# Kernel optimization log

Measured on AMD Instinct MI355X. Metric: run time of the kernel, lower is better.

The kernel has to match this reference:

```python
import jax, jax.numpy as jnp
import numpy as np

G, A = 1024, 20          # graphs, atoms per graph
N = G * A                # nodes = 20480
E = G * A * A            # fc edges within each graph = 409600
H = 128                  # hidden_dim
LATENT = 256             # latent_dim
L = 4                    # num_layers
NFREQ = 10
DIS_DIM = NFREQ * 2 * 3  # 60
EDGE_IN = 2 * H + 9 + DIS_DIM  # 325
MAX_ATOMS = 100


def _lin(k, fin, fout):
    return jax.random.normal(k, (fin, fout), dtype=jnp.float32) / np.sqrt(fin).astype(np.float32)


def _stack_lin(k, fin, fout):
    return jnp.stack([_lin(jax.random.fold_in(k, i), fin, fout) for i in range(L)])


def setup_inputs() -> dict:
    key = jax.random.key(0)
    ks = jax.random.split(key, 16)
    atom_types = jax.random.randint(ks[0], (N,), 0, MAX_ATOMS, dtype=jnp.int32)
    frac_coords = jax.random.uniform(ks[1], (N, 3), dtype=jnp.float32)
    lattices = jax.random.normal(ks[2], (G, 3, 3), dtype=jnp.float32)
    t = jax.random.normal(ks[3], (G, LATENT), dtype=jnp.float32)
    # fully-connected (fc) edges within each graph, block-diagonal structure
    base = np.arange(A)
    src = np.repeat(base, A)
    dst = np.tile(base, A)
    offs = (np.arange(G) * A)[:, None]
    edge_index = jnp.asarray(np.stack([
        (src[None, :] + offs).reshape(-1),
        (dst[None, :] + offs).reshape(-1)]), dtype=jnp.int32)  # [2, E]
    edge2graph = jnp.asarray(np.repeat(np.arange(G), A * A), dtype=jnp.int32)
    node2graph = jnp.asarray(np.repeat(np.arange(G), A), dtype=jnp.int32)
    # parameters
    emb_table = jax.random.normal(ks[4], (MAX_ATOMS, H), dtype=jnp.float32) * 0.02
    w_latent = _lin(ks[5], H + LATENT, H)
    b_latent = jnp.zeros((H,), jnp.float32)
    edge_w1 = _stack_lin(ks[6], EDGE_IN, H)
    edge_b1 = jnp.zeros((L, H), jnp.float32)
    edge_w2 = _stack_lin(ks[7], H, H)
    edge_b2 = jnp.zeros((L, H), jnp.float32)
    node_w1 = _stack_lin(ks[8], 2 * H, H)
    node_b1 = jnp.zeros((L, H), jnp.float32)
    node_w2 = _stack_lin(ks[9], H, H)
    node_b2 = jnp.zeros((L, H), jnp.float32)
    coord_w = _lin(ks[10], H, 3)
    lattice_w = _lin(ks[11], H, 9)
    return dict(atom_types=atom_types, frac_coords=frac_coords, lattices=lattices, t=t,
                edge_index=edge_index, edge2graph=edge2graph, node2graph=node2graph,
                emb_table=emb_table, w_latent=w_latent, b_latent=b_latent,
                edge_w1=edge_w1, edge_b1=edge_b1, edge_w2=edge_w2, edge_b2=edge_b2,
                node_w1=node_w1, node_b1=node_b1, node_w2=node_w2, node_b2=node_b2,
                coord_w=coord_w, lattice_w=lattice_w)


def reference(atom_types, frac_coords, lattices, t, edge_index, edge2graph, node2graph,
              emb_table, w_latent, b_latent,
              edge_w1, edge_b1, edge_w2, edge_b2,
              node_w1, node_b1, node_w2, node_b2,
              coord_w, lattice_w):
    silu = jax.nn.silu
    src, dst = edge_index[0], edge_index[1]
    # node embedding + latent conditioning
    h = emb_table[atom_types]                               # [N,H]
    h = jnp.concatenate([h, t[node2graph]], axis=1) @ w_latent + b_latent  # [N,H]
    # sinusoidal distance embedding of periodic frac diff (detached in original)
    frac_diff = (frac_coords[dst] - frac_coords[src]) % 1.0  # [E,3]
    freqs = 2.0 * jnp.pi * jnp.arange(NFREQ, dtype=frac_coords.dtype)
    emb = (frac_diff[..., None] * freqs).reshape(-1, 3 * NFREQ)
    dis = jax.lax.stop_gradient(jnp.concatenate([jnp.sin(emb), jnp.cos(emb)], axis=-1))  # [E,60]
    # lattice inner products, broadcast to edges (ip=True)
    lat_ip = jnp.einsum('gij,gkj->gik', lattices, lattices).reshape(-1, 9)
    lat_edges = lat_ip[edge2graph]                          # [E,9]
    # per-node edge counts for scatter-mean
    counts = jax.ops.segment_sum(jnp.ones_like(src, dtype=h.dtype), src, num_segments=N)
    inv_counts = (1.0 / jnp.maximum(counts, 1.0))[:, None]
    for i in range(L):
        e_in = jnp.concatenate([h[src], h[dst], lat_edges, dis], axis=1)  # [E,325]
        ef = silu(e_in @ edge_w1[i] + edge_b1[i])
        ef = silu(ef @ edge_w2[i] + edge_b2[i])               # [E,H]
        agg = jax.ops.segment_sum(ef, src, num_segments=N) * inv_counts   # scatter-mean
        n_in = jnp.concatenate([h, agg], axis=1)              # [N,2H]
        nf = silu(n_in @ node_w1[i] + node_b1[i])
        nf = silu(nf @ node_w2[i] + node_b2[i])
        h = h + nf                                            # residual
    coord_out = h @ coord_w                                   # [N,3]
    gcounts = jax.ops.segment_sum(jnp.ones((h.shape[0],), h.dtype), node2graph, num_segments=G)
    graph_feat = jax.ops.segment_sum(h, node2graph, num_segments=G) / gcounts[:, None]
    lattice_out = (graph_feat @ lattice_w).reshape(-1, 3, 3)
    lattice_out = jnp.einsum('bij,bjk->bik', lattice_out, lattices)  # ip=True
    return lattice_out, coord_out
```

## Files before the change

kernel.cpp:

```cpp
#include <hip/hip_runtime.h>
#include <stdint.h>


#define NA 20
#define HH 128

typedef unsigned short U16;
typedef unsigned int   U32;
typedef __attribute__((ext_vector_type(8))) short bf8;
typedef __attribute__((ext_vector_type(4))) float f4;

__device__ __forceinline__ float bf2f(U16 u){ return __uint_as_float(((U32)u)<<16); }
__device__ __forceinline__ U16 f2bf(float f){
    return (U16)((__float_as_uint(f) + 0x8000u) >> 16);
}
__device__ __forceinline__ float silu_f(float x){ return x/(1.0f+__expf(-x)); }
template<bool BF>
__device__ __forceinline__ float ldf(const void* p, long i){
    return BF ? bf2f(((const U16*)p)[i]) : ((const float*)p)[i];
}
__device__ __forceinline__ f4 mfma(bf8 a, bf8 b, f4 c){
    return __builtin_amdgcn_mfma_f32_16x16x32_bf16(a,b,c,0,0,0);
}
__device__ __forceinline__ bf8 ldsA(const U16* base, int stride, int row0,
                                    int kbase, int lrow, int quad){
    return *(const bf8*)(base + (row0+lrow)*stride + kbase + quad*8);
}
template<bool BF, bool WS>
__device__ __forceinline__ bf8 getB(const U16* wsb, long wbase, int kt, int nt,
                                    int lane, const void* W, long gbase, int N,
                                    int col, int kbase, int kmax, int quad){
    if constexpr(WS){
        return *(const bf8*)(wsb + wbase + (((long)kt*8 + nt)*64 + lane)*8);
    } else {
        bf8 b; int ks0 = kbase + quad*8;
#pragma unroll
        for(int j=0;j<8;j++){
            int k=ks0+j; U16 v=0;
            if(k<kmax) v = BF ? ((const U16*)W)[gbase+(long)k*N+col]
                              : f2bf(((const float*)W)[gbase+(long)k*N+col]);
            b[j]=(short)v;
        }
        return b;
    }
}

#define WS_LBASE(L) (49152 + (long)(L)*106496)
#define REPACK_BYTES 950272

__global__ __launch_bounds__(256) void repack(
    const void* wlat, const void* ew1, const void* ew2,
    const void* nw1p, const void* nw2p, const void* lat, U16* out)
{
    __shared__ int sG[4];
    const int tid=threadIdx.x;
    {
        const U16* l16=(const U16*)lat; int good=0;
#pragma unroll
        for(int u=0;u<32;u++){
            U16 x=l16[tid*32+u]; int e=(x>>7)&0xFF; good+=(e>=100&&e<=150)?1:0;
        }
#pragma unroll
        for(int o=32;o>0;o>>=1) good+=__shfl_xor(good,o);
        if((tid&63)==0) sG[tid>>6]=good;
    }
    __syncthreads();
    const bool bf = (sG[0]+sG[1]+sG[2]+sG[3]) > 6144;

    const void* W; long srow; int segk; long dst;
    const int ktg=blockIdx.x;
    if(ktg<12){ W=wlat; srow=(long)ktg*32; segk=32; dst=(long)ktg*4096; }
    else{
        int r=ktg-12, L=r/26, lk=r-26*L;
        dst = 49152 + (long)L*106496 + (long)lk*4096;
        if(lk<4)      { W=ew1;  srow=(long)L*325+lk*32;          segk=32; }
        else if(lk<8) { W=ew1;  srow=(long)L*325+128+(lk-4)*32;  segk=32; }
        else if(lk<10){ W=ew1;  srow=(long)L*325+265+(lk-8)*32;  segk=60-(lk-8)*32; }
        else if(lk<14){ W=ew2;  srow=(long)L*128+(lk-10)*32;     segk=32; }
        else if(lk<22){ W=nw1p; srow=(long)L*256+(lk-14)*32;     segk=32; }
        else          { W=nw2p; srow=(long)L*128+(lk-22)*32;     segk=32; }
    }
    for(int o=tid;o<4096;o+=256){
        int nt=o>>9, lane=(o>>3)&63, j=o&7;
        int kk=((lane>>4)<<3)+j, col=nt*16+(lane&15);
        U16 v=0;
        if(kk<segk){
            long idx=(srow+kk)*128+col;
            v = bf ? ((const U16*)W)[idx] : f2bf(((const float*)W)[idx]);
        }
        out[dst+o]=v;
    }
}

#define PB_OFF 8960
#define QB_OFF 11520
#define DB_OFF 14080
#define EB_OFF 19840

__device__ __forceinline__ void stage_dis(U16* dB, const float* tb, int ch, int tid){
    const float2* t2=(const float2*)tb;
#pragma unroll
    for(int it=0; it<5; ++it){
        int p = tid + it*512;
        int r = p>>5, j = p&31;
        if(j<30){
            int s = ch*4 + (r&3), d = r>>2;
            float2 vs = t2[s*30+j];
            float2 vd = t2[d*30+j];
            dB[r*72+j]    = f2bf(vd.x*vs.y - vd.y*vs.x);
            dB[r*72+j+30] = f2bf(vd.y*vs.y + vd.x*vs.x);
        }
    }
}

template<bool BF, bool WS>
__device__ void body(U16* sm, float* red, float* tb, float* Rall,
    const U16* wsb, int g, int tid,
    const int* __restrict__ atype, const void* frac, const void* lattices,
    const void* t, const void* emb, const void* wlat, const void* blat,
    const void* ew1, const void* eb1, const void* ew2, const void* eb2,
    const void* nw1p, const void* nb1, const void* nw2p, const void* nb2,
    const void* coordw, const void* latw, void* outv)
{
    const int lane=tid&63, w=tid>>6, lrow=lane&15, quad=lane>>4;
    const int c = w*16 + lrow;
    U16* HA=sm; U16* pB=sm+PB_OFF; U16* qB=sm+QB_OFF;
    U16* dB=sm+DB_OFF; U16* eB=sm+EB_OFF;
    U16* k1A=eB;
    float* tvecF=(float*)dB;

    for(int q=tid;q<2560;q+=512){
        int n=q>>7, cc=q&127;
        k1A[n*136+cc] = BF ? ((const U16*)emb)[(long)atype[g*NA+n]*HH+cc]
                           : f2bf(((const float*)emb)[(long)atype[g*NA+n]*HH+cc]);
    }
    for(int q=tid;q<600;q+=512){
        int n=q/30, jj=q-n*30;
        int dim=jj/10, f=jj-dim*10;
        float x = ldf<BF>(frac,(long)(g*NA+n)*3+dim);
        float rev = __builtin_amdgcn_fractf((float)f*x);
        float2 sc;
        sc.x=__builtin_amdgcn_sinf(rev);
        sc.y=__builtin_amdgcn_cosf(rev);
        ((float2*)tb)[q]=sc;
    }
    {
        int sl=tid>>7, j=tid&127; float acc=0.f;
        for(int kk=0;kk<64;kk++){
            int k=sl*64+kk;
            acc += ldf<BF>(t,(long)g*256+k)*ldf<BF>(wlat,(long)(HH+k)*HH+j);
        }
        tvecF[sl*128+j]=acc;
    }
    {
        int L=tid>>7, j=tid&127;
        float la[9];
#pragma unroll
        for(int m2=0;m2<9;m2++) la[m2]=ldf<BF>(lattices,(long)g*9+m2);
        float Rv=ldf<BF>(eb1,(long)L*HH+j);
        const long e1=(long)L*325*HH;
#pragma unroll
        for(int a2=0;a2<3;a2++)
#pragma unroll
        for(int b3=0;b3<3;b3++){
            float ip=0.f;
#pragma unroll
            for(int c2=0;c2<3;c2++) ip+=la[a2*3+c2]*la[b3*3+c2];
            Rv += ip*ldf<BF>(ew1, e1+(long)(256+a2*3+b3)*HH+j);
        }
        Rall[L*128+j]=Rv;
    }
    __syncthreads();
    {
        f4 a0={0.f,0.f,0.f,0.f}, a1={0.f,0.f,0.f,0.f};
#pragma unroll
        for(int ks=0;ks<4;ks++){
            bf8 b=getB<BF,WS>(wsb,0,ks,w,lane, wlat,0,HH,c,ks*32,128,quad);
            bf8 v0=ldsA(k1A,136,0,ks*32,lrow,quad);
            bf8 v1=ldsA(k1A,136,16,ks*32,lrow,quad);
            a0=mfma(v0,b,a0); a1=mfma(v1,b,a1);
        }
        float bias=ldf<BF>(blat,c)+tvecF[c]+tvecF[128+c]+tvecF[256+c]+tvecF[384+c];
#pragma unroll
        for(int r=0;r<4;r++){
            HA[(quad*4+r)*280+c]   =f2bf(a0[r]+bias);
            HA[(16+quad*4+r)*280+c]=f2bf(a1[r]+bias);
        }
    }
    __syncthreads();
    if(tid<320) dB[(tid>>2)*72+60+(tid&3)]=0;

    for(int L=0;L<4;L++){
        const long e1=(long)L*325*HH;
        const long LB=WS_LBASE(L);
        const int dir=L&1;
        {
            f4 p0={0.f,0.f,0.f,0.f}, p1={0.f,0.f,0.f,0.f};
            f4 q0={0.f,0.f,0.f,0.f}, q1={0.f,0.f,0.f,0.f};
#pragma unroll
            for(int ks=0;ks<4;ks++){
                bf8 bp=getB<BF,WS>(wsb,LB,      ks,w,lane, ew1,e1,       HH,c,ks*32,128,quad);
                bf8 bq=getB<BF,WS>(wsb,LB+16384,ks,w,lane, ew1,e1+128*HH,HH,c,ks*32,128,quad);
                bf8 v0=ldsA(HA,280,0,ks*32,lrow,quad);
                bf8 v1=ldsA(HA,280,16,ks*32,lrow,quad);
                p0=mfma(v0,bp,p0); p1=mfma(v1,bp,p1);
                q0=mfma(v0,bq,q0); q1=mfma(v1,bq,q1);
            }
            float Rc=Rall[L*128+c];
#pragma unroll
            for(int r=0;r<4;r++){
                int r0=quad*4+r, r1=16+quad*4+r;
                if(r0<20){ pB[r0*HH+c]=f2bf(p0[r]+Rc); qB[r0*HH+c]=f2bf(q0[r]); }
                if(r1<20){ pB[r1*HH+c]=f2bf(p1[r]+Rc); qB[r1*HH+c]=f2bf(q1[r]); }
            }
        }
        bf8 w1d0=getB<BF,WS>(wsb,LB+32768,0,w,lane, ew1,e1+(long)265*HH,HH,c,0, 60,quad);
        bf8 w1d1=getB<BF,WS>(wsb,LB+32768,1,w,lane, ew1,e1+(long)265*HH,HH,c,32,60,quad);
        bf8 w2f[4];
#pragma unroll
        for(int ks=0;ks<4;ks++)
            w2f[ks]=getB<BF,WS>(wsb,LB+40960,ks,w,lane, ew2,(long)L*HH*HH,HH,c,ks*32,128,quad);
        const float b2=ldf<BF>(eb2,(long)L*HH+c);
        if(L==0) stage_dis(dB,tb,0,tid);
        __syncthreads();

        for(int i=0;i<5;i++){
            const int ch = dir ? 4-i : i;
            float pv[4];
#pragma unroll
            for(int r=0;r<4;r++) pv[r]=bf2f(pB[(ch*4+r)*HH+c]);
#pragma unroll
            for(int m=0;m<5;m++){
                f4 a={0.f,0.f,0.f,0.f};
                __builtin_amdgcn_s_setprio(1);
                bf8 v0=ldsA(dB,72,m*16,0, lrow,quad);
                bf8 v1=ldsA(dB,72,m*16,32,lrow,quad);
                a=mfma(v0,w1d0,a); a=mfma(v1,w1d1,a);
                __builtin_amdgcn_s_setprio(0);
                float qd=bf2f(qB[(m*4+quad)*HH+c]);
#pragma unroll
                for(int r=0;r<4;r++){
                    int row=m*16+quad*4+r;
                    eB[row*136+c]=f2bf(silu_f(a[r]+pv[r]+qd));
                }
            }
            __syncthreads();
            if(i<4) stage_dis(dB,tb, dir?3-i:i+1, tid);
            float part[4]={0.f,0.f,0.f,0.f};
#pragma unroll
            for(int m=0;m<5;m++){
                f4 a={0.f,0.f,0.f,0.f};
                __builtin_amdgcn_s_setprio(1);
#pragma unroll
                for(int ks=0;ks<4;ks++){
                    bf8 v=ldsA(eB,136,m*16,ks*32,lrow,quad);
                    a=mfma(v,w2f[ks],a);
                }
                __builtin_amdgcn_s_setprio(0);
#pragma unroll
                for(int r=0;r<4;r++) part[r]+=silu_f(a[r]+b2);
            }
#pragma unroll
            for(int r=0;r<4;r++){
                float v=part[r];
                v+=__shfl_xor(v,16); v+=__shfl_xor(v,32);
                part[r]=v;
            }
            if(quad==0){
#pragma unroll
                for(int r=0;r<4;r++)
                    HA[(ch*4+r)*280+128+c]=f2bf(part[r]*0.05f);
            }
            __syncthreads();
        }
        {
            f4 a0={0.f,0.f,0.f,0.f}, a1={0.f,0.f,0.f,0.f};
#pragma unroll
            for(int ks=0;ks<8;ks++){
                bf8 b=getB<BF,WS>(wsb,LB+57344,ks,w,lane, nw1p,(long)L*256*HH,HH,c,ks*32,256,quad);
                bf8 v0=ldsA(HA,280,0,ks*32,lrow,quad);
                bf8 v1=ldsA(HA,280,16,ks*32,lrow,quad);
                a0=mfma(v0,b,a0); a1=mfma(v1,b,a1);
            }
            float n1=ldf<BF>(nb1,(long)L*HH+c);
#pragma unroll
            for(int r=0;r<4;r++){
                eB[(quad*4+r)*136+c]   =f2bf(silu_f(a0[r]+n1));
                eB[(16+quad*4+r)*136+c]=f2bf(silu_f(a1[r]+n1));
            }
        }
        __syncthreads();
        {
            f4 a0={0.f,0.f,0.f,0.f}, a1={0.f,0.f,0.f,0.f};
#pragma unroll
            for(int ks=0;ks<4;ks++){
                bf8 b=getB<BF,WS>(wsb,LB+90112,ks,w,lane, nw2p,(long)L*HH*HH,HH,c,ks*32,128,quad);
                bf8 v0=ldsA(eB,136,0,ks*32,lrow,quad);
                bf8 v1=ldsA(eB,136,16,ks*32,lrow,quad);
                a0=mfma(v0,b,a0); a1=mfma(v1,b,a1);
            }
            float n2=ldf<BF>(nb2,(long)L*HH+c);
#pragma unroll
            for(int r=0;r<4;r++){
                int r0=quad*4+r, r1=16+quad*4+r;
                HA[r0*280+c]=f2bf(bf2f(HA[r0*280+c])+silu_f(a0[r]+n2));
                HA[r1*280+c]=f2bf(bf2f(HA[r1*280+c])+silu_f(a1[r]+n2));
            }
        }
        __syncthreads();
    }

    {
        int o=tid>>3, l8=tid&7;
        float acc=0.f;
        int n=o/3, cc=o-n*3;
        if(o<60){
#pragma unroll
            for(int k8=0;k8<16;k8++){
                int k=l8*16+k8;
                acc += bf2f(HA[n*280+k]) * ldf<BF>(coordw,(long)k*3+cc);
            }
        }
        acc+=__shfl_xor(acc,1); acc+=__shfl_xor(acc,2); acc+=__shfl_xor(acc,4);
        if(o<60 && l8==0){
            if(BF) ((U16*)outv)[(long)1024*9+(long)(g*NA+n)*3+cc]=f2bf(acc);
            else   ((float*)outv)[(long)1024*9+(long)(g*NA+n)*3+cc]=acc;
        }
    }
    if(tid<HH){
        float s2=0.f;
        for(int n=0;n<NA;n++) s2+=bf2f(HA[n*280+tid]);
        red[tid]=s2*0.05f;
    }
    __syncthreads();
    {
        int o=tid>>4, l16=tid&15;
        float acc=0.f;
        if(o<9){
#pragma unroll
            for(int k8=0;k8<8;k8++){
                int k=l16*8+k8;
                acc += red[k]*ldf<BF>(latw,(long)k*9+o);
            }
        }
        acc+=__shfl_xor(acc,1); acc+=__shfl_xor(acc,2);
        acc+=__shfl_xor(acc,4); acc+=__shfl_xor(acc,8);
        if(o<9 && l16==0) red[HH+o]=acc;
    }
    __syncthreads();
    if(tid<9){
        int i2=tid/3, k2=tid-(tid/3)*3; float acc=0.f;
#pragma unroll
        for(int j3=0;j3<3;j3++)
            acc+=red[HH+i2*3+j3]*ldf<BF>(lattices,(long)g*9+j3*3+k2);
        if(BF) ((U16*)outv)[(long)g*9+tid]=f2bf(acc);
        else   ((float*)outv)[(long)g*9+tid]=acc;
    }
}

template<bool WS>
__device__ void mega_impl(const U16* wsb,
    const int* atype, const void* frac, const void* lattices, const void* t,
    const void* emb, const void* wlat, const void* blat,
    const void* ew1, const void* eb1, const void* ew2, const void* eb2,
    const void* nw1p, const void* nb1, const void* nw2p, const void* nb2,
    const void* coordw, const void* latw, void* outv)
{
    __shared__ __align__(16) unsigned char smraw[68928];
    U16* sm = (U16*)smraw;
    float* red = (float*)(smraw+61440);
    float* tb  = (float*)(smraw+62080);
    float* Rall= (float*)(smraw+66880);
    const int g=blockIdx.x, tid=threadIdx.x, w=tid>>6, lane=tid&63;
    int* di=(int*)red;
    {
        const U16* l16=(const U16*)lattices; int good=0;
#pragma unroll
        for(int u=0;u<16;u++){
            U16 x=l16[tid*16+u]; int e=(x>>7)&0xFF; good+=(e>=100&&e<=150)?1:0;
        }
#pragma unroll
        for(int o=32;o>0;o>>=1) good+=__shfl_xor(good,o);
        if(lane==0) di[w]=good;
    }
    __syncthreads();
    if(tid==0){ int s=0; for(int i=0;i<8;i++) s+=di[i]; di[8]=(s>6144)?1:0; }
    __syncthreads();
    const int bfm=di[8];
    __syncthreads();
    if(bfm) body<true ,WS>(sm,red,tb,Rall,wsb,g,tid,atype,frac,lattices,t,emb,wlat,blat,
                           ew1,eb1,ew2,eb2,nw1p,nb1,nw2p,nb2,coordw,latw,outv);
    else    body<false,WS>(sm,red,tb,Rall,wsb,g,tid,atype,frac,lattices,t,emb,wlat,blat,
                           ew1,eb1,ew2,eb2,nw1p,nb1,nw2p,nb2,coordw,latw,outv);
}

__global__ __launch_bounds__(512,2) void mega_ws(const U16* wsb,
    const int* atype, const void* frac, const void* lattices, const void* t,
    const void* emb, const void* wlat, const void* blat,
    const void* ew1, const void* eb1, const void* ew2, const void* eb2,
    const void* nw1p, const void* nb1, const void* nw2p, const void* nb2,
    const void* coordw, const void* latw, void* outv)
{
    mega_impl<true>(wsb,atype,frac,lattices,t,emb,wlat,blat,ew1,eb1,ew2,eb2,
                    nw1p,nb1,nw2p,nb2,coordw,latw,outv);
}

__global__ __launch_bounds__(512,2) void mega_direct(const U16* wsb,
    const int* atype, const void* frac, const void* lattices, const void* t,
    const void* emb, const void* wlat, const void* blat,
    const void* ew1, const void* eb1, const void* ew2, const void* eb2,
    const void* nw1p, const void* nb1, const void* nw2p, const void* nb2,
    const void* coordw, const void* latw, void* outv)
{
    mega_impl<false>(wsb,atype,frac,lattices,t,emb,wlat,blat,ew1,eb1,ew2,eb2,
                     nw1p,nb1,nw2p,nb2,coordw,latw,outv);
}

extern "C" void kernel_launch(void* const* d_in, const int* in_sizes, int n_in,
                              void* d_out, int out_size, void* d_ws, size_t ws_size,
                              hipStream_t stream)
{
    (void)in_sizes; (void)n_in; (void)out_size;
    const int* atype = (const int*)d_in[0];
    if(ws_size >= REPACK_BYTES){
        repack<<<116, 256, 0, stream>>>(d_in[8], d_in[10], d_in[12], d_in[14],
                                        d_in[16], d_in[2], (U16*)d_ws);
        mega_ws<<<1024, 512, 0, stream>>>((const U16*)d_ws,
            atype, d_in[1], d_in[2], d_in[3], d_in[7], d_in[8], d_in[9],
            d_in[10], d_in[11], d_in[12], d_in[13], d_in[14], d_in[15],
            d_in[16], d_in[17], d_in[18], d_in[19], d_out);
    } else {
        mega_direct<<<1024, 512, 0, stream>>>(nullptr,
            atype, d_in[1], d_in[2], d_in[3], d_in[7], d_in[8], d_in[9],
            d_in[10], d_in[11], d_in[12], d_in[13], d_in[14], d_in[15],
            d_in[16], d_in[17], d_in[18], d_in[19], d_out);
    }
}
```

Before: 397.3 us.

## Keep p/q projections in registers and halve edge buffer to raise occupancy

Removes the pB/qB LDS staging buffers, keeping per-node projections in registers and distributing them with cross-lane shuffles. The 80-row edge tile per chunk is split into two sub-tiles of 48 and 32 rows so the eB buffer shrinks, cutting shared memory from about 69KB to about 50KB. Launch bounds are raised from 2 to 6 blocks per SIMD group to allow more resident blocks. In exchange the kernel adds barriers and shuffles per chunk, and the tighter register budget risks spills.

```diff
diff --git a/kernel.cpp b/kernel.cpp
--- a/kernel.cpp
+++ b/kernel.cpp
@@ -92,10 +92,8 @@
     }
 }
 
-#define PB_OFF 8960
-#define QB_OFF 11520
-#define DB_OFF 14080
-#define EB_OFF 19840
+#define DB_OFF 8960
+#define EB_OFF 14720
 
 __device__ __forceinline__ void stage_dis(U16* dB, const float* tb, int ch, int tid){
     const float2* t2=(const float2*)tb;
@@ -124,8 +122,7 @@
 {
     const int lane=tid&63, w=tid>>6, lrow=lane&15, quad=lane>>4;
     const int c = w*16 + lrow;
-    U16* HA=sm; U16* pB=sm+PB_OFF; U16* qB=sm+QB_OFF;
-    U16* dB=sm+DB_OFF; U16* eB=sm+EB_OFF;
+    U16* HA=sm; U16* dB=sm+DB_OFF; U16* eB=sm+EB_OFF;
     U16* k1A=eB;
     float* tvecF=(float*)dB;
 
@@ -194,6 +191,7 @@
         const long e1=(long)L*325*HH;
         const long LB=WS_LBASE(L);
         const int dir=L&1;
+        float p0f[4],p1f[4],q0f[4],q1f[4];
         {
             f4 p0={0.f,0.f,0.f,0.f}, p1={0.f,0.f,0.f,0.f};
             f4 q0={0.f,0.f,0.f,0.f}, q1={0.f,0.f,0.f,0.f};
@@ -209,10 +207,21 @@
             float Rc=Rall[L*128+c];
 #pragma unroll
             for(int r=0;r<4;r++){
-                int r0=quad*4+r, r1=16+quad*4+r;
-                if(r0<20){ pB[r0*HH+c]=f2bf(p0[r]+Rc); qB[r0*HH+c]=f2bf(q0[r]); }
-                if(r1<20){ pB[r1*HH+c]=f2bf(p1[r]+Rc); qB[r1*HH+c]=f2bf(q1[r]); }
-            }
+                p0f[r]=p0[r]+Rc; p1f[r]=p1[r]+Rc;
+                q0f[r]=q0[r];    q1f[r]=q1[r];
+            }
+        }
+        float qreg[5];
+#pragma unroll
+        for(int m=0;m<4;m++){
+            float t0=__shfl(q0f[0], m*16+lrow), t1=__shfl(q0f[1], m*16+lrow);
+            float t2=__shfl(q0f[2], m*16+lrow), t3=__shfl(q0f[3], m*16+lrow);
+            qreg[m] = (quad&2) ? ((quad&1)?t3:t2) : ((quad&1)?t1:t0);
+        }
+        {
+            float t0=__shfl(q1f[0], lrow), t1=__shfl(q1f[1], lrow);
+            float t2=__shfl(q1f[2], lrow), t3=__shfl(q1f[3], lrow);
+            qreg[4] = (quad&2) ? ((quad&1)?t3:t2) : ((quad&1)?t1:t0);
         }
         bf8 w1d0=getB<BF,WS>(wsb,LB+32768,0,w,lane, ew1,e1+(long)265*HH,HH,c,0, 60,quad);
         bf8 w1d1=getB<BF,WS>(wsb,LB+32768,1,w,lane, ew1,e1+(long)265*HH,HH,c,32,60,quad);
@@ -221,23 +230,28 @@
         for(int ks=0;ks<4;ks++)
             w2f[ks]=getB<BF,WS>(wsb,LB+40960,ks,w,lane, ew2,(long)L*HH*HH,HH,c,ks*32,128,quad);
         const float b2=ldf<BF>(eb2,(long)L*HH+c);
-        if(L==0) stage_dis(dB,tb,0,tid);
-        __syncthreads();
+        if(L==0){ stage_dis(dB,tb,0,tid); __syncthreads(); }
 
         for(int i=0;i<5;i++){
             const int ch = dir ? 4-i : i;
             float pv[4];
-#pragma unroll
-            for(int r=0;r<4;r++) pv[r]=bf2f(pB[(ch*4+r)*HH+c]);
-#pragma unroll
-            for(int m=0;m<5;m++){
+            if(ch<4){
+#pragma unroll
+                for(int r=0;r<4;r++) pv[r]=__shfl(p0f[r], ch*16+lrow);
+            } else {
+#pragma unroll
+                for(int r=0;r<4;r++) pv[r]=__shfl(p1f[r], lrow);
+            }
+            float part[4]={0.f,0.f,0.f,0.f};
+#pragma unroll
+            for(int m=0;m<3;m++){
                 f4 a={0.f,0.f,0.f,0.f};
                 __builtin_amdgcn_s_setprio(1);
                 bf8 v0=ldsA(dB,72,m*16,0, lrow,quad);
                 bf8 v1=ldsA(dB,72,m*16,32,lrow,quad);
                 a=mfma(v0,w1d0,a); a=mfma(v1,w1d1,a);
                 __builtin_amdgcn_s_setprio(0);
-                float qd=bf2f(qB[(m*4+quad)*HH+c]);
+                float qd=qreg[m];
 #pragma unroll
                 for(int r=0;r<4;r++){
                     int row=m*16+quad*4+r;
@@ -245,10 +259,8 @@
                 }
             }
             __syncthreads();
-            if(i<4) stage_dis(dB,tb, dir?3-i:i+1, tid);
-            float part[4]={0.f,0.f,0.f,0.f};
-#pragma unroll
-            for(int m=0;m<5;m++){
+#pragma unroll
+            for(int m=0;m<3;m++){
                 f4 a={0.f,0.f,0.f,0.f};
                 __builtin_amdgcn_s_setprio(1);
 #pragma unroll
@@ -260,6 +272,37 @@
 #pragma unroll
                 for(int r=0;r<4;r++) part[r]+=silu_f(a[r]+b2);
             }
+            __syncthreads();
+#pragma unroll
+            for(int m=3;m<5;m++){
+                f4 a={0.f,0.f,0.f,0.f};
+                __builtin_amdgcn_s_setprio(1);
+                bf8 v0=ldsA(dB,72,m*16,0, lrow,quad);
+                bf8 v1=ldsA(dB,72,m*16,32,lrow,quad);
+                a=mfma(v0,w1d0,a); a=mfma(v1,w1d1,a);
+                __builtin_amdgcn_s_setprio(0);
+                float qd=qreg[m];
+#pragma unroll
+                for(int r=0;r<4;r++){
+                    int row=(m-3)*16+quad*4+r;
+                    eB[row*136+c]=f2bf(silu_f(a[r]+pv[r]+qd));
+                }
+            }
+            __syncthreads();
+#pragma unroll
+            for(int m=3;m<5;m++){
+                f4 a={0.f,0.f,0.f,0.f};
+                __builtin_amdgcn_s_setprio(1);
+#pragma unroll
+                for(int ks=0;ks<4;ks++){
+                    bf8 v=ldsA(eB,136,(m-3)*16,ks*32,lrow,quad);
+                    a=mfma(v,w2f[ks],a);
+                }
+                __builtin_amdgcn_s_setprio(0);
+#pragma unroll
+                for(int r=0;r<4;r++) part[r]+=silu_f(a[r]+b2);
+            }
+            if(i<4) stage_dis(dB,tb, dir?3-i:i+1, tid);
 #pragma unroll
             for(int r=0;r<4;r++){
                 float v=part[r];
@@ -366,11 +409,11 @@
     const void* nw1p, const void* nb1, const void* nw2p, const void* nb2,
     const void* coordw, const void* latw, void* outv)
 {
-    __shared__ __align__(16) unsigned char smraw[68928];
+    __shared__ __align__(16) unsigned char smraw[49984];
     U16* sm = (U16*)smraw;
-    float* red = (float*)(smraw+61440);
-    float* tb  = (float*)(smraw+62080);
-    float* Rall= (float*)(smraw+66880);
+    float* red = (float*)(smraw+42496);
+    float* tb  = (float*)(smraw+43136);
+    float* Rall= (float*)(smraw+47936);
     const int g=blockIdx.x, tid=threadIdx.x, w=tid>>6, lane=tid&63;
     int* di=(int*)red;
     {
@@ -394,7 +437,7 @@
                            ew1,eb1,ew2,eb2,nw1p,nb1,nw2p,nb2,coordw,latw,outv);
 }
 
-__global__ __launch_bounds__(512,2) void mega_ws(const U16* wsb,
+__global__ __launch_bounds__(512,6) void mega_ws(const U16* wsb,
     const int* atype, const void* frac, const void* lattices, const void* t,
     const void* emb, const void* wlat, const void* blat,
     const void* ew1, const void* eb1, const void* ew2, const void* eb2,
@@ -405,7 +448,7 @@
                     nw1p,nb1,nw2p,nb2,coordw,latw,outv);
 }
 
-__global__ __launch_bounds__(512,2) void mega_direct(const U16* wsb,
+__global__ __launch_bounds__(512,6) void mega_direct(const U16* wsb,
     const int* atype, const void* frac, const void* lattices, const void* t,
     const void* emb, const void* wlat, const void* blat,
     const void* ew1, const void* eb1, const void* ew2, const void* eb2,
```

Result: slower. 460.0 us (+15.8%).

## Split edge chunk processing in two halves to shrink LDS footprint

Applied to the files above, without the earlier changes.

The per-chunk edge MLP now runs in two halves (3 then 2 row tiles) that reuse a smaller eB staging buffer, and the HA/pB/qB regions are trimmed to 20 rows instead of 32. Total shared memory drops from about 67KB to about 52KB. The aim is to fit more workgroups per CU for better latency hiding. The cost is two extra __syncthreads per chunk, and the next dis staging now happens later, after the second half.

```diff
diff --git a/kernel.cpp b/kernel.cpp
--- a/kernel.cpp
+++ b/kernel.cpp
@@ -92,10 +92,10 @@
     }
 }
 
-#define PB_OFF 8960
-#define QB_OFF 11520
-#define DB_OFF 14080
-#define EB_OFF 19840
+#define PB_OFF 5600
+#define QB_OFF 8160
+#define DB_OFF 10720
+#define EB_OFF 16480
 
 __device__ __forceinline__ void stage_dis(U16* dB, const float* tb, int ch, int tid){
     const float2* t2=(const float2*)tb;
@@ -183,8 +183,9 @@
         float bias=ldf<BF>(blat,c)+tvecF[c]+tvecF[128+c]+tvecF[256+c]+tvecF[384+c];
 #pragma unroll
         for(int r=0;r<4;r++){
-            HA[(quad*4+r)*280+c]   =f2bf(a0[r]+bias);
-            HA[(16+quad*4+r)*280+c]=f2bf(a1[r]+bias);
+            int r1=16+quad*4+r;
+            HA[(quad*4+r)*280+c]=f2bf(a0[r]+bias);
+            if(r1<20) HA[r1*280+c]=f2bf(a1[r]+bias);
         }
     }
     __syncthreads();
@@ -210,7 +211,7 @@
 #pragma unroll
             for(int r=0;r<4;r++){
                 int r0=quad*4+r, r1=16+quad*4+r;
-                if(r0<20){ pB[r0*HH+c]=f2bf(p0[r]+Rc); qB[r0*HH+c]=f2bf(q0[r]); }
+                pB[r0*HH+c]=f2bf(p0[r]+Rc); qB[r0*HH+c]=f2bf(q0[r]);
                 if(r1<20){ pB[r1*HH+c]=f2bf(p1[r]+Rc); qB[r1*HH+c]=f2bf(q1[r]); }
             }
         }
@@ -229,8 +230,9 @@
             float pv[4];
 #pragma unroll
             for(int r=0;r<4;r++) pv[r]=bf2f(pB[(ch*4+r)*HH+c]);
-#pragma unroll
-            for(int m=0;m<5;m++){
+            float part[4]={0.f,0.f,0.f,0.f};
+#pragma unroll
+            for(int m=0;m<3;m++){
                 f4 a={0.f,0.f,0.f,0.f};
                 __builtin_amdgcn_s_setprio(1);
                 bf8 v0=ldsA(dB,72,m*16,0, lrow,quad);
@@ -245,10 +247,8 @@
                 }
             }
             __syncthreads();
-            if(i<4) stage_dis(dB,tb, dir?3-i:i+1, tid);
-            float part[4]={0.f,0.f,0.f,0.f};
-#pragma unroll
-            for(int m=0;m<5;m++){
+#pragma unroll
+            for(int m=0;m<3;m++){
                 f4 a={0.f,0.f,0.f,0.f};
                 __builtin_amdgcn_s_setprio(1);
 #pragma unroll
@@ -260,6 +260,37 @@
 #pragma unroll
                 for(int r=0;r<4;r++) part[r]+=silu_f(a[r]+b2);
             }
+            __syncthreads();
+#pragma unroll
+            for(int m=3;m<5;m++){
+                f4 a={0.f,0.f,0.f,0.f};
+                __builtin_amdgcn_s_setprio(1);
+                bf8 v0=ldsA(dB,72,m*16,0, lrow,quad);
+                bf8 v1=ldsA(dB,72,m*16,32,lrow,quad);
+                a=mfma(v0,w1d0,a); a=mfma(v1,w1d1,a);
+                __builtin_amdgcn_s_setprio(0);
+                float qd=bf2f(qB[(m*4+quad)*HH+c]);
+#pragma unroll
+                for(int r=0;r<4;r++){
+                    int row=(m-3)*16+quad*4+r;
+                    eB[row*136+c]=f2bf(silu_f(a[r]+pv[r]+qd));
+                }
+            }
+            __syncthreads();
+#pragma unroll
+            for(int m=3;m<5;m++){
+                f4 a={0.f,0.f,0.f,0.f};
+                __builtin_amdgcn_s_setprio(1);
+#pragma unroll
+                for(int ks=0;ks<4;ks++){
+                    bf8 v=ldsA(eB,136,(m-3)*16,ks*32,lrow,quad);
+                    a=mfma(v,w2f[ks],a);
+                }
+                __builtin_amdgcn_s_setprio(0);
+#pragma unroll
+                for(int r=0;r<4;r++) part[r]+=silu_f(a[r]+b2);
+            }
+            if(i<4) stage_dis(dB,tb, dir?3-i:i+1, tid);
 #pragma unroll
             for(int r=0;r<4;r++){
                 float v=part[r];
@@ -304,7 +335,7 @@
             for(int r=0;r<4;r++){
                 int r0=quad*4+r, r1=16+quad*4+r;
                 HA[r0*280+c]=f2bf(bf2f(HA[r0*280+c])+silu_f(a0[r]+n2));
-                HA[r1*280+c]=f2bf(bf2f(HA[r1*280+c])+silu_f(a1[r]+n2));
+                if(r1<20) HA[r1*280+c]=f2bf(bf2f(HA[r1*280+c])+silu_f(a1[r]+n2));
             }
         }
         __syncthreads();
@@ -366,11 +397,11 @@
     const void* nw1p, const void* nb1, const void* nw2p, const void* nb2,
     const void* coordw, const void* latw, void* outv)
 {
-    __shared__ __align__(16) unsigned char smraw[68928];
+    __shared__ __align__(16) unsigned char smraw[53504];
     U16* sm = (U16*)smraw;
-    float* red = (float*)(smraw+61440);
-    float* tb  = (float*)(smraw+62080);
-    float* Rall= (float*)(smraw+66880);
+    float* red = (float*)(smraw+46016);
+    float* tb  = (float*)(smraw+46656);
+    float* Rall= (float*)(smraw+51456);
     const int g=blockIdx.x, tid=threadIdx.x, w=tid>>6, lane=tid&63;
     int* di=(int*)red;
     {
```

After: 414.1 us. 1.04x slower.
